# Performance work log

Measured on AMD Instinct MI355X. Metric: run time of the kernel, lower is better.

Reference implementation:

```python
import jax, jax.numpy as jnp
import numpy as np

N_NODES = 100000
NFEAT, NHID, NCLASS, HEADS = 256, 16, 40, 8
NEG_SLOPE = 0.2


def gat_conv(x, src, dst, W, att_src, att_dst, bias, n_nodes):
    """PyG-style GATConv (concat heads). x:[N,Fin], src/dst:[E] (self-loops included)."""
    H, C = att_src.shape
    h = (x @ W).reshape(n_nodes, H, C)                      # [N,H,C]
    a_src = jnp.einsum('nhc,hc->nh', h, att_src)            # [N,H]
    a_dst = jnp.einsum('nhc,hc->nh', h, att_dst)            # [N,H]
    e = jax.nn.leaky_relu(a_src[src] + a_dst[dst], NEG_SLOPE)  # [E,H]
    # segment softmax over edges grouped by destination node
    emax = jax.ops.segment_max(e, dst, num_segments=n_nodes)
    emax = jnp.where(jnp.isfinite(emax), emax, 0.0)
    ex = jnp.exp(e - emax[dst])
    denom = jax.ops.segment_sum(ex, dst, num_segments=n_nodes)
    alpha = ex / (denom[dst] + 1e-16)                       # [E,H]
    msg = h[src] * alpha[:, :, None]                        # [E,H,C] gather + weight
    out = jax.ops.segment_sum(msg, dst, num_segments=n_nodes)  # [N,H,C]
    return out.reshape(n_nodes, H * C) + bias


def setup_inputs() -> dict:
    key = jax.random.key(0)
    ks = jax.random.split(key, 12)
    E = 1600000
    x = jax.random.normal(ks[0], (N_NODES, NFEAT), dtype=jnp.float32)
    edge_index = jax.random.randint(ks[1], (2, E), 0, N_NODES, dtype=jnp.int64)
    s = 0.05
    W1 = jax.random.normal(ks[2], (NFEAT, HEADS * NHID), dtype=jnp.float32) * s
    att_src1 = jax.random.normal(ks[3], (HEADS, NHID), dtype=jnp.float32) * s
    att_dst1 = jax.random.normal(ks[4], (HEADS, NHID), dtype=jnp.float32) * s
    b1 = jnp.zeros((HEADS * NHID,), dtype=jnp.float32)
    W2 = jax.random.normal(ks[5], (HEADS * NHID, NCLASS), dtype=jnp.float32) * s
    att_src2 = jax.random.normal(ks[6], (1, NCLASS), dtype=jnp.float32) * s
    att_dst2 = jax.random.normal(ks[7], (1, NCLASS), dtype=jnp.float32) * s
    b2 = jnp.zeros((NCLASS,), dtype=jnp.float32)
    return {"x": x, "edge_index": edge_index, "W1": W1, "att_src1": att_src1,
            "att_dst1": att_dst1, "b1": b1, "W2": W2, "att_src2": att_src2,
            "att_dst2": att_dst2, "b2": b2}


def reference(x, edge_index, W1, att_src1, att_dst1, b1, W2, att_src2, att_dst2, b2):
    n = x.shape[0]
    # PyG GATConv adds self-loops by default
    loop = jnp.arange(n, dtype=edge_index.dtype)
    src = jnp.concatenate([edge_index[0], loop])
    dst = jnp.concatenate([edge_index[1], loop])
    h = gat_conv(x, src, dst, W1, att_src1, att_dst1, b1, n)
    h = jax.nn.relu(h)  # activation='relu'; dropout/bn are identity in eval / use_bn=False
    out = gat_conv(h, src, dst, W2, att_src2, att_dst2, b2, n)
    return out
```

## Files before the change

kernel.cpp:

```cpp
#include <hip/hip_runtime.h>
#include <math.h>

#define KF 256
#define F1 128
#define NH 8
#define NC 16
#define NCLS 40
#define NEG 0.2f
#define BM 64

static __device__ __forceinline__ float lrelu(float v) { return fmaxf(v, NEG * v); }

static __device__ __forceinline__ unsigned bf16r(float a) {
    unsigned u = __float_as_uint(a);
    return (u + 0x7fffu + ((u >> 16) & 1u)) >> 16;
}
static __device__ __forceinline__ unsigned bf16pack2(float a, float b) {
    return bf16r(a) | (bf16r(b) << 16);
}
static __device__ __forceinline__ float2 bf2unpack(unsigned v) {
    float2 r;
    r.x = __uint_as_float(v << 16);
    r.y = __uint_as_float(v & 0xffff0000u);
    return r;
}

typedef __attribute__((ext_vector_type(8))) short bf16x8;
typedef __attribute__((ext_vector_type(4))) float f32x4;

union pk8 { uint4 u; bf16x8 v; };

__global__ __launch_bounds__(256) void wprep_kernel(const float* __restrict__ W1,
                                                    unsigned short* __restrict__ wfrag)
{
    int gid = blockIdx.x * 256 + threadIdx.x;
    if (gid >= KF * F1) return;
    int k = gid >> 7, nn = gid & 127;
    int kt = k >> 6, ks = (k >> 5) & 1, oct = (k >> 3) & 3, e = k & 7;
    int nt = nn >> 4, ln = (nn & 15) + 16 * oct;
    int idx = (((kt * 8 + nt) * 2 + ks) * 64 + ln) * 8 + e;
    wfrag[idx] = (unsigned short)bf16r(W1[gid]);
}

__global__ __launch_bounds__(256) void gemm1_kernel(const float* __restrict__ x,
        const unsigned short* __restrict__ wfrag,
        const float* __restrict__ att_src, const float* __restrict__ att_dst,
        unsigned short* __restrict__ h1u, float* __restrict__ a_src, float* __restrict__ a_dst, int n)
{
    __shared__ __align__(16) unsigned short Bl[32768];
    const int t = threadIdx.x;
    const int w = t >> 6, lane = t & 63;
    const int row0 = blockIdx.x * BM;

    {
        const uint4* src = (const uint4*)wfrag;
        uint4* dstp = (uint4*)Bl;
#pragma unroll
        for (int i = 0; i < 16; ++i) dstp[t + i * 256] = src[t + i * 256];
    }
    __syncthreads();

    const int m = lane & 15, kq = lane >> 4;
    const int row = row0 + w * 16 + m;
    const bool rv = row < n;
    const float* xr = x + (size_t)(rv ? row : row0) * KF + kq * 8;
    const float4 z4 = make_float4(0.f, 0.f, 0.f, 0.f);

    f32x4 acc[8];
#pragma unroll
    for (int i = 0; i < 8; ++i) acc[i] = (f32x4){0.f, 0.f, 0.f, 0.f};

#pragma unroll
    for (int kt = 0; kt < 4; ++kt) {
        float4 xa = rv ? *(const float4*)&xr[kt * 64]          : z4;
        float4 xb = rv ? *(const float4*)&xr[kt * 64 + 4]      : z4;
        float4 xc = rv ? *(const float4*)&xr[kt * 64 + 32]     : z4;
        float4 xd = rv ? *(const float4*)&xr[kt * 64 + 32 + 4] : z4;
        pk8 pa, pb;
        pa.u = make_uint4(bf16pack2(xa.x, xa.y), bf16pack2(xa.z, xa.w),
                          bf16pack2(xb.x, xb.y), bf16pack2(xb.z, xb.w));
        pb.u = make_uint4(bf16pack2(xc.x, xc.y), bf16pack2(xc.z, xc.w),
                          bf16pack2(xd.x, xd.y), bf16pack2(xd.z, xd.w));
#pragma unroll
        for (int nt = 0; nt < 8; ++nt) {
            bf16x8 b0 = *(const bf16x8*)&Bl[(((kt * 8 + nt) * 2 + 0) * 64 + lane) * 8];
            bf16x8 b1 = *(const bf16x8*)&Bl[(((kt * 8 + nt) * 2 + 1) * 64 + lane) * 8];
            acc[nt] = __builtin_amdgcn_mfma_f32_16x16x32_bf16(pa.v, b0, acc[nt], 0, 0, 0);
            acc[nt] = __builtin_amdgcn_mfma_f32_16x16x32_bf16(pb.v, b1, acc[nt], 0, 0, 0);
        }
    }

    const int col = lane & 15, g = lane >> 4;
    const int rbase = row0 + w * 16 + g * 4;
#pragma unroll
    for (int nt = 0; nt < 8; ++nt) {
        float asv = att_src[nt * 16 + col];
        float adv = att_dst[nt * 16 + col];
#pragma unroll
        for (int reg = 0; reg < 4; ++reg) {
            int orow = rbase + reg;
            float hv = acc[nt][reg];
            if (orow < n) h1u[(size_t)orow * F1 + nt * 16 + col] = (unsigned short)bf16r(hv);
            float ps = hv * asv, pd = hv * adv;
            ps += __shfl_xor(ps, 1); ps += __shfl_xor(ps, 2);
            ps += __shfl_xor(ps, 4); ps += __shfl_xor(ps, 8);
            pd += __shfl_xor(pd, 1); pd += __shfl_xor(pd, 2);
            pd += __shfl_xor(pd, 4); pd += __shfl_xor(pd, 8);
            if (col == 0 && orow < n) {
                a_src[orow * NH + nt] = ps;
                a_dst[orow * NH + nt] = pd;
            }
        }
    }
}

__global__ __launch_bounds__(256) void histrank_kernel(const int* __restrict__ ei, int E, int Etot,
                                                       int* __restrict__ counts,
                                                       int* __restrict__ rank)
{
    const int base = blockIdx.x * 2048 + threadIdx.x;
#pragma unroll
    for (int q = 0; q < 8; ++q) {
        int i = base + q * 256;
        if (i < Etot) {
            int dst = (i < E) ? ei[E + i] : (i - E);
            rank[i] = atomicAdd(&counts[dst], 1);
        }
    }
}

__global__ __launch_bounds__(256) void scan1_kernel(const int* __restrict__ counts,
                                                    int* __restrict__ bsum, int n)
{
    __shared__ int lds[256];
    const int t = threadIdx.x;
    const int base = blockIdx.x * 1024 + t * 4;
    int s = 0;
#pragma unroll
    for (int q = 0; q < 4; ++q) { int i = base + q; if (i < n) s += counts[i]; }
    lds[t] = s;
    __syncthreads();
#pragma unroll
    for (int off = 128; off > 0; off >>= 1) {
        if (t < off) lds[t] += lds[t + off];
        __syncthreads();
    }
    if (t == 0) bsum[blockIdx.x] = lds[0];
}

__global__ __launch_bounds__(256) void scan2_kernel(const int* __restrict__ bsum,
                                                    int* __restrict__ boffs, int nb,
                                                    int* __restrict__ indptr, int n, int Etot)
{
    __shared__ int lds[256];
    const int t = threadIdx.x;
    lds[t] = (t < nb) ? bsum[t] : 0;
    __syncthreads();
    for (int off = 1; off < 256; off <<= 1) {
        int v = (t >= off) ? lds[t - off] : 0;
        __syncthreads();
        lds[t] += v;
        __syncthreads();
    }
    if (t < nb) boffs[t] = (t == 0) ? 0 : lds[t - 1];
    if (t == 0) indptr[n] = Etot;
}

__global__ __launch_bounds__(256) void scan3_kernel(const int* __restrict__ counts,
                                                    const int* __restrict__ boffs,
                                                    int* __restrict__ indptr, int n)
{
    __shared__ int lds[256];
    const int t = threadIdx.x;
    const int base = blockIdx.x * 1024 + t * 4;
    int c[4];
    int s = 0;
#pragma unroll
    for (int q = 0; q < 4; ++q) {
        int i = base + q;
        c[q] = (i < n) ? counts[i] : 0;
        s += c[q];
    }
    lds[t] = s;
    __syncthreads();
    for (int off = 1; off < 256; off <<= 1) {
        int v = (t >= off) ? lds[t - off] : 0;
        __syncthreads();
        lds[t] += v;
        __syncthreads();
    }
    int run = boffs[blockIdx.x] + lds[t] - s;
#pragma unroll
    for (int q = 0; q < 4; ++q) {
        int i = base + q;
        if (i < n) indptr[i] = run;
        run += c[q];
    }
}

__global__ __launch_bounds__(256) void fill_kernel(const int* __restrict__ ei, int E, int Etot,
                                                   const int* __restrict__ indptr,
                                                   const int* __restrict__ rank,
                                                   int* __restrict__ sorted_src)
{
    const int base = blockIdx.x * 2048 + threadIdx.x;
#pragma unroll
    for (int q = 0; q < 8; ++q) {
        int i = base + q * 256;
        if (i < Etot) {
            int src, dst;
            if (i < E) { src = ei[i]; dst = ei[E + i]; }
            else       { src = i - E; dst = i - E; }
            sorted_src[indptr[dst] + rank[i]] = src;
        }
    }
}

__global__ __launch_bounds__(256) void agg1_kernel(const unsigned* __restrict__ h1b,
        const float* __restrict__ a_src, const float* __restrict__ a_dst,
        const int* __restrict__ indptr, const int* __restrict__ ssrc,
        const float* __restrict__ b1, unsigned* __restrict__ out1b, int n)
{
    const int wave = threadIdx.x >> 6, lane = threadIdx.x & 63;
    const int dst = blockIdx.x * 4 + wave;
    if (dst >= n) return;
    const int h = lane >> 3;
    const float ad = a_dst[dst * NH + h];
    const int beg = indptr[dst], end = indptr[dst + 1];
    float s0 = 0.f, s1 = 0.f, s2 = 0.f, s3 = 0.f;
    float ax0 = 0.f, ay0 = 0.f, ax1 = 0.f, ay1 = 0.f;
    float ax2 = 0.f, ay2 = 0.f, ax3 = 0.f, ay3 = 0.f;
    int j = beg;
    for (; j + 4 <= end; j += 4) {
        int sc0 = ssrc[j], sc1 = ssrc[j + 1], sc2 = ssrc[j + 2], sc3 = ssrc[j + 3];
        float as0 = a_src[sc0 * NH + h];
        float as1 = a_src[sc1 * NH + h];
        float as2 = a_src[sc2 * NH + h];
        float as3 = a_src[sc3 * NH + h];
        unsigned v0 = h1b[(size_t)sc0 * 64 + lane];
        unsigned v1 = h1b[(size_t)sc1 * 64 + lane];
        unsigned v2 = h1b[(size_t)sc2 * 64 + lane];
        unsigned v3 = h1b[(size_t)sc3 * 64 + lane];
        float p0 = __expf(lrelu(as0 + ad));
        float p1 = __expf(lrelu(as1 + ad));
        float p2 = __expf(lrelu(as2 + ad));
        float p3 = __expf(lrelu(as3 + ad));
        float2 hv0 = bf2unpack(v0), hv1 = bf2unpack(v1);
        float2 hv2 = bf2unpack(v2), hv3 = bf2unpack(v3);
        s0 += p0; ax0 += p0 * hv0.x; ay0 += p0 * hv0.y;
        s1 += p1; ax1 += p1 * hv1.x; ay1 += p1 * hv1.y;
        s2 += p2; ax2 += p2 * hv2.x; ay2 += p2 * hv2.y;
        s3 += p3; ax3 += p3 * hv3.x; ay3 += p3 * hv3.y;
    }
    for (; j < end; ++j) {
        int sc = ssrc[j];
        float as = a_src[sc * NH + h];
        float2 hv = bf2unpack(h1b[(size_t)sc * 64 + lane]);
        float p = __expf(lrelu(as + ad));
        s0 += p; ax0 += p * hv.x; ay0 += p * hv.y;
    }
    float s = (s0 + s1) + (s2 + s3);
    float accx = (ax0 + ax1) + (ax2 + ax3);
    float accy = (ay0 + ay1) + (ay2 + ay3);
    float inv = 1.f / (s + 1e-16f);
    float2 bb = *(const float2*)&b1[lane * 2];
    float ox = fmaxf(accx * inv + bb.x, 0.f);
    float oy = fmaxf(accy * inv + bb.y, 0.f);
    out1b[(size_t)dst * 64 + lane] = bf16pack2(ox, oy);
}

__global__ __launch_bounds__(256) void gemm2_kernel(const unsigned* __restrict__ out1b,
        const float* __restrict__ W2, const float* __restrict__ atts2,
        const float* __restrict__ attd2,
        unsigned short* __restrict__ h2us, float* __restrict__ a_src, float* __restrict__ a_dst, int n)
{
    __shared__ float wl[128][NCLS];
    __shared__ float xs[64][68];
    const int t = threadIdx.x;
    const int row0 = blockIdx.x * 64;
    const int rg = t >> 3;
    const int cg = t & 7;
    const int r0 = rg * 2;

#pragma unroll
    for (int i = t; i < 1280; i += 256)
        *(float4*)&wl[0][0 + i * 4] = *(const float4*)&W2[i * 4];

    float acc[2][5];
#pragma unroll
    for (int i = 0; i < 2; ++i)
#pragma unroll
        for (int j = 0; j < 5; ++j) acc[i][j] = 0.f;

    for (int kh = 0; kh < 2; ++kh) {
#pragma unroll
        for (int i = t; i < 1024; i += 256) {
            int r = i >> 4, u2 = i & 15;
            int gr = row0 + r;
            float4 v = make_float4(0.f, 0.f, 0.f, 0.f);
            if (gr < n) {
                uint2 pk = *(const uint2*)&out1b[(size_t)gr * 64 + kh * 32 + u2 * 2];
                float2 ab = bf2unpack(pk.x);
                float2 cd = bf2unpack(pk.y);
                v = make_float4(ab.x, ab.y, cd.x, cd.y);
            }
            *(float4*)&xs[r][u2 * 4] = v;
        }
        __syncthreads();
#pragma unroll 4
        for (int k = 0; k < 64; ++k) {
            float xa = xs[r0][k];
            float xb = xs[r0 + 1][k];
            const float* wr = &wl[kh * 64 + k][cg * 5];
#pragma unroll
            for (int j = 0; j < 5; ++j) {
                float w = wr[j];
                acc[0][j] += xa * w;
                acc[1][j] += xb * w;
            }
        }
        __syncthreads();
    }

    float as5[5], ad5[5];
#pragma unroll
    for (int j = 0; j < 5; ++j) {
        as5[j] = atts2[cg * 5 + j];
        ad5[j] = attd2[cg * 5 + j];
    }
#pragma unroll
    for (int i = 0; i < 2; ++i) {
        int row = row0 + r0 + i;
        if (row >= n) break;
#pragma unroll
        for (int j = 0; j < 5; ++j)
            h2us[(size_t)row * NCLS + cg * 5 + j] = (unsigned short)bf16r(acc[i][j]);
        float ps = acc[i][0] * as5[0] + acc[i][1] * as5[1] + acc[i][2] * as5[2]
                 + acc[i][3] * as5[3] + acc[i][4] * as5[4];
        float pd = acc[i][0] * ad5[0] + acc[i][1] * ad5[1] + acc[i][2] * ad5[2]
                 + acc[i][3] * ad5[3] + acc[i][4] * ad5[4];
        ps += __shfl_xor(ps, 1); ps += __shfl_xor(ps, 2); ps += __shfl_xor(ps, 4);
        pd += __shfl_xor(pd, 1); pd += __shfl_xor(pd, 2); pd += __shfl_xor(pd, 4);
        if (cg == 0) { a_src[row] = ps; a_dst[row] = pd; }
    }
}

__global__ __launch_bounds__(256) void agg2_kernel(const unsigned* __restrict__ h2b,
        const float* __restrict__ a_src, const float* __restrict__ a_dst,
        const int* __restrict__ indptr, const int* __restrict__ ssrc,
        const float* __restrict__ b2, float* __restrict__ out, int n)
{
    const int wave = threadIdx.x >> 6, lane = threadIdx.x & 63;
    const int grp = lane / 20;
    const int sub = lane - grp * 20;
    const int dst = blockIdx.x * 12 + wave * 3 + grp;
    const bool valid = (grp < 3) && (dst < n);
    const float ad = valid ? a_dst[dst] : 0.f;
    int beg = 0, end = 0;
    if (valid) { beg = indptr[dst]; end = indptr[dst + 1]; }
    float s0 = 0.f, s1 = 0.f, s2 = 0.f, s3 = 0.f;
    float ax0 = 0.f, ay0 = 0.f, ax1 = 0.f, ay1 = 0.f;
    float ax2 = 0.f, ay2 = 0.f, ax3 = 0.f, ay3 = 0.f;
    int j = beg;
    for (; j + 4 <= end; j += 4) {
        int sc0 = ssrc[j], sc1 = ssrc[j + 1], sc2 = ssrc[j + 2], sc3 = ssrc[j + 3];
        float p0 = __expf(lrelu(a_src[sc0] + ad));
        float p1 = __expf(lrelu(a_src[sc1] + ad));
        float p2 = __expf(lrelu(a_src[sc2] + ad));
        float p3 = __expf(lrelu(a_src[sc3] + ad));
        float2 h0 = bf2unpack(h2b[(size_t)sc0 * 20 + sub]);
        float2 h1v = bf2unpack(h2b[(size_t)sc1 * 20 + sub]);
        float2 h2v = bf2unpack(h2b[(size_t)sc2 * 20 + sub]);
        float2 h3v = bf2unpack(h2b[(size_t)sc3 * 20 + sub]);
        s0 += p0; ax0 += p0 * h0.x;  ay0 += p0 * h0.y;
        s1 += p1; ax1 += p1 * h1v.x; ay1 += p1 * h1v.y;
        s2 += p2; ax2 += p2 * h2v.x; ay2 += p2 * h2v.y;
        s3 += p3; ax3 += p3 * h3v.x; ay3 += p3 * h3v.y;
    }
    for (; j < end; ++j) {
        int sc = ssrc[j];
        float p = __expf(lrelu(a_src[sc] + ad));
        float2 hv = bf2unpack(h2b[(size_t)sc * 20 + sub]);
        s0 += p; ax0 += p * hv.x; ay0 += p * hv.y;
    }
    if (valid) {
        float s = (s0 + s1) + (s2 + s3);
        float accx = (ax0 + ax1) + (ax2 + ax3);
        float accy = (ay0 + ay1) + (ay2 + ay3);
        float inv = 1.f / (s + 1e-16f);
        float2 o;
        o.x = accx * inv + b2[sub * 2];
        o.y = accy * inv + b2[sub * 2 + 1];
        *(float2*)&out[(size_t)dst * NCLS + sub * 2] = o;
    }
}

extern "C" void kernel_launch(void* const* d_in, const int* in_sizes, int n_in,
                              void* d_out, int out_size, void* d_ws, size_t ws_size,
                              hipStream_t stream)
{
    const float* x   = (const float*)d_in[0];
    const int*   ei  = (const int*)d_in[1];
    const float* W1  = (const float*)d_in[2];
    const float* as1 = (const float*)d_in[3];
    const float* ad1 = (const float*)d_in[4];
    const float* b1  = (const float*)d_in[5];
    const float* W2  = (const float*)d_in[6];
    const float* as2 = (const float*)d_in[7];
    const float* ad2 = (const float*)d_in[8];
    const float* b2  = (const float*)d_in[9];
    float* out = (float*)d_out;

    const int n    = in_sizes[0] / KF;
    const int E    = in_sizes[1] / 2;
    const int Etot = E + n;

    char* ws = (char*)d_ws;
    unsigned* h1b   = (unsigned*)ws;
    unsigned* out1b = (unsigned*)(ws + 25600000);
    float* a_s1     = (float*)(ws + 51200000);
    float* a_d1     = (float*)(ws + 54400000);
    int*   indptr   = (int*)  (ws + 57600000);
    int*   counts   = (int*)  (ws + 58000016);
    int*   ssrc     = (int*)  (ws + 58400016);
    unsigned short* wfrag = (unsigned short*)(ws + 65200016);
    int*   rank     = (int*)  (ws + 65270016);
    int*   bsum     = (int*)  (ws + 72070016);
    int*   boffs    = (int*)  (ws + 72074112);
    unsigned* h2b   = (unsigned*)ws;
    float* a_s2     = (float*)(ws + 8000000);
    float* a_d2     = (float*)(ws + 8400000);

    const int nb = (n + 1023) / 1024;
    dim3 b256(256);

    hipMemsetAsync(counts, 0, n * sizeof(int), stream);
    wprep_kernel<<<dim3((KF * F1 + 255) / 256), b256, 0, stream>>>(W1, wfrag);
    gemm1_kernel<<<dim3((n + BM - 1) / BM), b256, 0, stream>>>(x, wfrag, as1, ad1,
                                                               (unsigned short*)h1b, a_s1, a_d1, n);
    histrank_kernel<<<dim3((Etot + 2047) / 2048), b256, 0, stream>>>(ei, E, Etot, counts, rank);
    scan1_kernel<<<dim3(nb), b256, 0, stream>>>(counts, bsum, n);
    scan2_kernel<<<dim3(1), b256, 0, stream>>>(bsum, boffs, nb, indptr, n, Etot);
    scan3_kernel<<<dim3(nb), b256, 0, stream>>>(counts, boffs, nb ? indptr : indptr, n);
    fill_kernel<<<dim3((Etot + 2047) / 2048), b256, 0, stream>>>(ei, E, Etot, indptr, rank, ssrc);
    agg1_kernel<<<dim3((n + 3) / 4), b256, 0, stream>>>(h1b, a_s1, a_d1, indptr, ssrc, b1, out1b, n);
    gemm2_kernel<<<dim3((n + 63) / 64), b256, 0, stream>>>(out1b, W2, as2, ad2,
                                                           (unsigned short*)h2b, a_s2, a_d2, n);
    agg2_kernel<<<dim3((n + 11) / 12), b256, 0, stream>>>(h2b, a_s2, a_d2, indptr, ssrc, b2, out, n);
}
```

Measured before the change: 355.1 us.

## Retile gemm1 so each wave owns two column tiles and reads B from global

gemm1 no longer stages the full 64KB bf16 weight fragment in shared memory per block. Each block now handles 32 rows, and each of its four waves computes two 16-column tiles for both 16-row groups, loading its B fragments straight from global memory (L2-resident). This removes the per-block 64KB LDS copy and the barrier, and the freed LDS lets more blocks be resident. In exchange, every wave re-reads the x rows (4x redundant x loads within a block), which could add traffic on a memory-bound GEMM.

```diff
diff --git a/kernel.cpp b/kernel.cpp
--- a/kernel.cpp
+++ b/kernel.cpp
@@ -7,7 +7,6 @@
 #define NC 16
 #define NCLS 40
 #define NEG 0.2f
-#define BM 64
 
 static __device__ __forceinline__ float lrelu(float v) { return fmaxf(v, NEG * v); }
 
@@ -47,68 +46,80 @@
         const float* __restrict__ att_src, const float* __restrict__ att_dst,
         unsigned short* __restrict__ h1u, float* __restrict__ a_src, float* __restrict__ a_dst, int n)
 {
-    __shared__ __align__(16) unsigned short Bl[32768];
     const int t = threadIdx.x;
     const int w = t >> 6, lane = t & 63;
-    const int row0 = blockIdx.x * BM;
-
-    {
-        const uint4* src = (const uint4*)wfrag;
-        uint4* dstp = (uint4*)Bl;
-#pragma unroll
-        for (int i = 0; i < 16; ++i) dstp[t + i * 256] = src[t + i * 256];
-    }
-    __syncthreads();
+    const int row0 = blockIdx.x * 32;
+    const int nt0 = w * 2;
 
     const int m = lane & 15, kq = lane >> 4;
-    const int row = row0 + w * 16 + m;
-    const bool rv = row < n;
-    const float* xr = x + (size_t)(rv ? row : row0) * KF + kq * 8;
+    const int rA = row0 + m, rB = rA + 16;
+    const bool vA = rA < n, vB = rB < n;
+    const float* xA = x + (size_t)(vA ? rA : 0) * KF + kq * 8;
+    const float* xB = x + (size_t)(vB ? rB : 0) * KF + kq * 8;
     const float4 z4 = make_float4(0.f, 0.f, 0.f, 0.f);
 
-    f32x4 acc[8];
-#pragma unroll
-    for (int i = 0; i < 8; ++i) acc[i] = (f32x4){0.f, 0.f, 0.f, 0.f};
+    f32x4 acc[2][2];
+#pragma unroll
+    for (int i = 0; i < 2; ++i)
+#pragma unroll
+        for (int j = 0; j < 2; ++j) acc[i][j] = (f32x4){0.f, 0.f, 0.f, 0.f};
 
 #pragma unroll
     for (int kt = 0; kt < 4; ++kt) {
-        float4 xa = rv ? *(const float4*)&xr[kt * 64]          : z4;
-        float4 xb = rv ? *(const float4*)&xr[kt * 64 + 4]      : z4;
-        float4 xc = rv ? *(const float4*)&xr[kt * 64 + 32]     : z4;
-        float4 xd = rv ? *(const float4*)&xr[kt * 64 + 32 + 4] : z4;
-        pk8 pa, pb;
-        pa.u = make_uint4(bf16pack2(xa.x, xa.y), bf16pack2(xa.z, xa.w),
-                          bf16pack2(xb.x, xb.y), bf16pack2(xb.z, xb.w));
-        pb.u = make_uint4(bf16pack2(xc.x, xc.y), bf16pack2(xc.z, xc.w),
-                          bf16pack2(xd.x, xd.y), bf16pack2(xd.z, xd.w));
-#pragma unroll
-        for (int nt = 0; nt < 8; ++nt) {
-            bf16x8 b0 = *(const bf16x8*)&Bl[(((kt * 8 + nt) * 2 + 0) * 64 + lane) * 8];
-            bf16x8 b1 = *(const bf16x8*)&Bl[(((kt * 8 + nt) * 2 + 1) * 64 + lane) * 8];
-            acc[nt] = __builtin_amdgcn_mfma_f32_16x16x32_bf16(pa.v, b0, acc[nt], 0, 0, 0);
-            acc[nt] = __builtin_amdgcn_mfma_f32_16x16x32_bf16(pb.v, b1, acc[nt], 0, 0, 0);
-        }
+        bf16x8 B00 = *(const bf16x8*)&wfrag[(((kt * 8 + nt0    ) * 2 + 0) * 64 + lane) * 8];
+        bf16x8 B01 = *(const bf16x8*)&wfrag[(((kt * 8 + nt0    ) * 2 + 1) * 64 + lane) * 8];
+        bf16x8 B10 = *(const bf16x8*)&wfrag[(((kt * 8 + nt0 + 1) * 2 + 0) * 64 + lane) * 8];
+        bf16x8 B11 = *(const bf16x8*)&wfrag[(((kt * 8 + nt0 + 1) * 2 + 1) * 64 + lane) * 8];
+        float4 a0 = vA ? *(const float4*)&xA[kt * 64]      : z4;
+        float4 a1 = vA ? *(const float4*)&xA[kt * 64 + 4]  : z4;
+        float4 a2 = vA ? *(const float4*)&xA[kt * 64 + 32] : z4;
+        float4 a3 = vA ? *(const float4*)&xA[kt * 64 + 36] : z4;
+        float4 b0 = vB ? *(const float4*)&xB[kt * 64]      : z4;
+        float4 b1 = vB ? *(const float4*)&xB[kt * 64 + 4]  : z4;
+        float4 b2 = vB ? *(const float4*)&xB[kt * 64 + 32] : z4;
+        float4 b3 = vB ? *(const float4*)&xB[kt * 64 + 36] : z4;
+        pk8 pAa, pAb, pBa, pBb;
+        pAa.u = make_uint4(bf16pack2(a0.x, a0.y), bf16pack2(a0.z, a0.w),
+                           bf16pack2(a1.x, a1.y), bf16pack2(a1.z, a1.w));
+        pAb.u = make_uint4(bf16pack2(a2.x, a2.y), bf16pack2(a2.z, a2.w),
+                           bf16pack2(a3.x, a3.y), bf16pack2(a3.z, a3.w));
+        pBa.u = make_uint4(bf16pack2(b0.x, b0.y), bf16pack2(b0.z, b0.w),
+                           bf16pack2(b1.x, b1.y), bf16pack2(b1.z, b1.w));
+        pBb.u = make_uint4(bf16pack2(b2.x, b2.y), bf16pack2(b2.z, b2.w),
+                           bf16pack2(b3.x, b3.y), bf16pack2(b3.z, b3.w));
+        acc[0][0] = __builtin_amdgcn_mfma_f32_16x16x32_bf16(pAa.v, B00, acc[0][0], 0, 0, 0);
+        acc[0][0] = __builtin_amdgcn_mfma_f32_16x16x32_bf16(pAb.v, B01, acc[0][0], 0, 0, 0);
+        acc[0][1] = __builtin_amdgcn_mfma_f32_16x16x32_bf16(pAa.v, B10, acc[0][1], 0, 0, 0);
+        acc[0][1] = __builtin_amdgcn_mfma_f32_16x16x32_bf16(pAb.v, B11, acc[0][1], 0, 0, 0);
+        acc[1][0] = __builtin_amdgcn_mfma_f32_16x16x32_bf16(pBa.v, B00, acc[1][0], 0, 0, 0);
+        acc[1][0] = __builtin_amdgcn_mfma_f32_16x16x32_bf16(pBb.v, B01, acc[1][0], 0, 0, 0);
+        acc[1][1] = __builtin_amdgcn_mfma_f32_16x16x32_bf16(pBa.v, B10, acc[1][1], 0, 0, 0);
+        acc[1][1] = __builtin_amdgcn_mfma_f32_16x16x32_bf16(pBb.v, B11, acc[1][1], 0, 0, 0);
     }
 
     const int col = lane & 15, g = lane >> 4;
-    const int rbase = row0 + w * 16 + g * 4;
-#pragma unroll
-    for (int nt = 0; nt < 8; ++nt) {
-        float asv = att_src[nt * 16 + col];
-        float adv = att_dst[nt * 16 + col];
-#pragma unroll
-        for (int reg = 0; reg < 4; ++reg) {
-            int orow = rbase + reg;
-            float hv = acc[nt][reg];
-            if (orow < n) h1u[(size_t)orow * F1 + nt * 16 + col] = (unsigned short)bf16r(hv);
-            float ps = hv * asv, pd = hv * adv;
-            ps += __shfl_xor(ps, 1); ps += __shfl_xor(ps, 2);
-            ps += __shfl_xor(ps, 4); ps += __shfl_xor(ps, 8);
-            pd += __shfl_xor(pd, 1); pd += __shfl_xor(pd, 2);
-            pd += __shfl_xor(pd, 4); pd += __shfl_xor(pd, 8);
-            if (col == 0 && orow < n) {
-                a_src[orow * NH + nt] = ps;
-                a_dst[orow * NH + nt] = pd;
+#pragma unroll
+    for (int rg = 0; rg < 2; ++rg) {
+        const int rbase = row0 + rg * 16 + g * 4;
+#pragma unroll
+        for (int ntl = 0; ntl < 2; ++ntl) {
+            const int nt = nt0 + ntl;
+            float asv = att_src[nt * 16 + col];
+            float adv = att_dst[nt * 16 + col];
+#pragma unroll
+            for (int reg = 0; reg < 4; ++reg) {
+                int row = rbase + reg;
+                float hv = acc[rg][ntl][reg];
+                if (row < n) h1u[(size_t)row * F1 + nt * 16 + col] = (unsigned short)bf16r(hv);
+                float ps = hv * asv, pd = hv * adv;
+                ps += __shfl_xor(ps, 1); ps += __shfl_xor(ps, 2);
+                ps += __shfl_xor(ps, 4); ps += __shfl_xor(ps, 8);
+                pd += __shfl_xor(pd, 1); pd += __shfl_xor(pd, 2);
+                pd += __shfl_xor(pd, 4); pd += __shfl_xor(pd, 8);
+                if (col == 0 && row < n) {
+                    a_src[row * NH + nt] = ps;
+                    a_dst[row * NH + nt] = pd;
+                }
             }
         }
     }
@@ -436,12 +447,12 @@
 
     hipMemsetAsync(counts, 0, n * sizeof(int), stream);
     wprep_kernel<<<dim3((KF * F1 + 255) / 256), b256, 0, stream>>>(W1, wfrag);
-    gemm1_kernel<<<dim3((n + BM - 1) / BM), b256, 0, stream>>>(x, wfrag, as1, ad1,
-                                                               (unsigned short*)h1b, a_s1, a_d1, n);
+    gemm1_kernel<<<dim3((n + 31) / 32), b256, 0, stream>>>(x, wfrag, as1, ad1,
+                                                           (unsigned short*)h1b, a_s1, a_d1, n);
     histrank_kernel<<<dim3((Etot + 2047) / 2048), b256, 0, stream>>>(ei, E, Etot, counts, rank);
     scan1_kernel<<<dim3(nb), b256, 0, stream>>>(counts, bsum, n);
     scan2_kernel<<<dim3(1), b256, 0, stream>>>(bsum, boffs, nb, indptr, n, Etot);
-    scan3_kernel<<<dim3(nb), b256, 0, stream>>>(counts, boffs, nb ? indptr : indptr, n);
+    scan3_kernel<<<dim3(nb), b256, 0, stream>>>(counts, boffs, indptr, n);
     fill_kernel<<<dim3((Etot + 2047) / 2048), b256, 0, stream>>>(ei, E, Etot, indptr, rank, ssrc);
     agg1_kernel<<<dim3((n + 3) / 4), b256, 0, stream>>>(h1b, a_s1, a_d1, indptr, ssrc, b1, out1b, n);
     gemm2_kernel<<<dim3((n + 63) / 64), b256, 0, stream>>>(out1b, W2, as2, ad2,
```

Measured after the change: 467.5 us. +31.6%, slower.
